# Kernel optimization log

Measured on AMD Instinct MI355X. Metric: run time of the kernel, lower is better.

Reference implementation:

```python
import jax, jax.numpy as jnp
import numpy as np

NUM_BINS = 256


def _per_channel_hist(img):
    # img: [B, C, H, W] with histc range [0, 1].
    B, C, H, W = img.shape
    x = jnp.transpose(img, (1, 0, 2, 3)).reshape(C, -1)  # [C, N]
    # torch.histc: bin = floor(x * bins); value == max goes to last bin;
    # values outside [min, max] are ignored.
    idx = jnp.clip(jnp.floor(x * NUM_BINS).astype(jnp.int32), 0, NUM_BINS - 1)
    valid = ((x >= 0.0) & (x <= 1.0)).astype(img.dtype)  # [C, N]
    offsets = (jnp.arange(C, dtype=jnp.int32) * NUM_BINS)[:, None]
    flat_idx = (idx + offsets).reshape(-1)
    hist = jax.ops.segment_sum(valid.reshape(-1), flat_idx,
                               num_segments=C * NUM_BINS)
    return hist.reshape(C, NUM_BINS)


def setup_inputs() -> dict:
    key = jax.random.key(0)
    k1, k2 = jax.random.split(key)
    img1 = jax.random.uniform(k1, (16, 3, 512, 512), dtype=jnp.float32)
    img2 = jax.random.uniform(k2, (16, 3, 512, 512), dtype=jnp.float32)
    return {"img1": img1, "img2": img2}


def reference(img1, img2):
    h1 = _per_channel_hist(img1)  # [C, bins]
    h2 = _per_channel_hist(img2)
    h1 = h1 / jnp.sum(h1, axis=1, keepdims=True)
    h2 = h2 / jnp.sum(h2, axis=1, keepdims=True)
    cdf1 = jnp.cumsum(h1, axis=1)
    cdf2 = jnp.cumsum(h2, axis=1)
    loss = jnp.sum(jnp.abs(cdf1 - cdf2))  # sum over channels and bins
    return loss / 3.0
```

## Files before the change

kernel.cpp:

```cpp
#include <hip/hip_runtime.h>

#define NUM_BINS 256
#define HW4 65536
#define NGROUPS 6
#define BPG 512
#define GRID (NGROUPS * BPG)
#define THREADS 64
#define F4_PER_BLOCK 2048
#define BATCHES 16
#define ROWS_ALLOC 272

__global__ __launch_bounds__(THREADS) void hist_kernel(
    const float* __restrict__ img1,
    const float* __restrict__ img2,
    unsigned int* __restrict__ ghist ) {

    __shared__ unsigned char h8[ROWS_ALLOC * 64];

    const int lane = threadIdx.x;

    uint4* z = (uint4*)h8;
    #pragma unroll
    for (int i = 0; i < 17; ++i)
        z[i * THREADS + lane] = make_uint4(0u, 0u, 0u, 0u);
    __syncthreads();

    const int gid = blockIdx.x;
    const int group = gid >> 9;
    const int blk = gid & (BPG - 1);
    const int im = (group >= 3) ? 1 : 0;
    const int c = group - im * 3;
    const int b = blk >> 5;
    const int joff = (blk & 31) * F4_PER_BLOCK;
    const float4* __restrict__ src =
        (const float4*)(im ? img2 : img1) + (size_t)(b * 3 + c) * HW4 + joff + lane;

    float4 va = src[0];
    float4 vb = src[THREADS];

    for (int it = 0; it < BATCHES; ++it) {
        float4 na, nb;
        if (it + 1 < BATCHES) {
            na = src[(it + 1) * 2 * THREADS];
            nb = src[(it + 1) * 2 * THREADS + THREADS];
        }

        const float xs[8] = {va.x, va.y, va.z, va.w, vb.x, vb.y, vb.z, vb.w};
        int row[8];
        #pragma unroll
        for (int e = 0; e < 8; ++e) {
            const float x = xs[e];
            int bi = (int)(x * 256.0f);
            bi = bi > (NUM_BINS - 1) ? (NUM_BINS - 1) : bi;
            row[e] = (x >= 0.0f && x <= 1.0f) ? bi : 256;
        }

        unsigned inc[8], dead[8];
        #pragma unroll
        for (int e = 0; e < 8; ++e) { inc[e] = 1u; dead[e] = 0u; }
        #pragma unroll
        for (int i = 0; i < 8; ++i)
            #pragma unroll
            for (int j = i + 1; j < 8; ++j) {
                const unsigned e = (row[i] == row[j]) ? 1u : 0u;
                inc[i] += e;
                dead[j] |= e;
            }

        unsigned v[8];
        #pragma unroll
        for (int e = 0; e < 8; ++e)
            v[e] = h8[(row[e] << 6) | lane];
        #pragma unroll
        for (int e = 0; e < 8; ++e)
            if (!dead[e])
                h8[(row[e] << 6) | lane] = (unsigned char)(v[e] + inc[e]);

        va = na; vb = nb;
    }
    __syncthreads();

    #pragma unroll
    for (int q = 0; q < 4; ++q) {
        const int bin = (q << 6) | lane;
        const unsigned* rowp = (const unsigned*)&h8[bin << 6];
        unsigned s = 0;
        #pragma unroll
        for (int w = 0; w < 16; ++w) {
            const unsigned x = rowp[(w + (lane >> 1)) & 15];
            s += (x & 0xffu) + ((x >> 8) & 0xffu) + ((x >> 16) & 0xffu)
               + (x >> 24);
        }
        if (s) atomicAdd(&ghist[group * NUM_BINS + bin], s);
    }
}

__global__ __launch_bounds__(NUM_BINS) void finalize_kernel(
    const unsigned int* __restrict__ hist, float* __restrict__ out) {

    __shared__ float b1[NUM_BINS];
    __shared__ float b2[NUM_BINS];
    __shared__ float red[NUM_BINS / 64];

    const int t = threadIdx.x;
    float acc = 0.0f;

    for (int c = 0; c < 3; ++c) {
        b1[t] = (float)hist[c * NUM_BINS + t];
        b2[t] = (float)hist[(3 + c) * NUM_BINS + t];
        __syncthreads();
        for (int off = 1; off < NUM_BINS; off <<= 1) {
            float a1 = 0.0f, a2 = 0.0f;
            if (t >= off) { a1 = b1[t - off]; a2 = b2[t - off]; }
            __syncthreads();
            b1[t] += a1;
            b2[t] += a2;
            __syncthreads();
        }
        acc += fabsf(b1[t] / b1[NUM_BINS - 1] - b2[t] / b2[NUM_BINS - 1]);
        __syncthreads();
    }

    #pragma unroll
    for (int off = 32; off > 0; off >>= 1)
        acc += __shfl_down(acc, off, 64);
    if ((t & 63) == 0) red[t >> 6] = acc;
    __syncthreads();
    if (t == 0)
        out[0] = (red[0] + red[1] + red[2] + red[3]) * (1.0f / 3.0f);
}

extern "C" void kernel_launch(void* const* d_in, const int* in_sizes, int n_in,
                              void* d_out, int out_size, void* d_ws,
                              size_t ws_size, hipStream_t stream) {
    const float* img1 = (const float*)d_in[0];
    const float* img2 = (const float*)d_in[1];
    float* out = (float*)d_out;
    unsigned int* hist = (unsigned int*)d_ws;

    hipMemsetAsync(hist, 0, NGROUPS * NUM_BINS * sizeof(unsigned int), stream);

    hist_kernel<<<GRID, THREADS, 0, stream>>>(img1, img2, hist);
    finalize_kernel<<<1, NUM_BINS, 0, stream>>>(hist, out);
}
```

Measured before the change: 140.8 us.

## Use 2D grid with strided chunk distribution, deeper prefetch, and interleaved bin layout

The flat grid of 3072 blocks becomes a 426x6 grid in which each block walks chunks strided by the block count, so each block handles about 20 iterations and fewer blocks are launched. Prefetch depth goes from one to two iterations to hide more load latency. The shared byte histogram pairs adjacent bins per lane so the histogram drops the spill row and fits in 16KB, and out-of-range values now add zero instead of landing in an extra row. The final reduction reads 32 words per stripe and emits two bins each. Uneven per-block work (19 vs 20 iterations) and the extra register pressure are the tradeoffs; 20 increments per lane still fits in an 8-bit counter.

After: 154.7 us. 1.1x slower.

```diff
diff --git a/kernel.cpp b/kernel.cpp
--- a/kernel.cpp
+++ b/kernel.cpp
@@ -3,95 +3,105 @@
 #define NUM_BINS 256
 #define HW4 65536
 #define NGROUPS 6
-#define BPG 512
-#define GRID (NGROUPS * BPG)
+#define BPG 426
+#define CHUNKS 8192
 #define THREADS 64
-#define F4_PER_BLOCK 2048
-#define BATCHES 16
-#define ROWS_ALLOC 272
+#define MAXIT 20
 
 __global__ __launch_bounds__(THREADS) void hist_kernel(
     const float* __restrict__ img1,
     const float* __restrict__ img2,
     unsigned int* __restrict__ ghist ) {
 
-    __shared__ unsigned char h8[ROWS_ALLOC * 64];
+    __shared__ unsigned char h8[16384];
 
     const int lane = threadIdx.x;
+    const int lane2 = lane << 1;
 
     uint4* z = (uint4*)h8;
     #pragma unroll
-    for (int i = 0; i < 17; ++i)
+    for (int i = 0; i < 16; ++i)
         z[i * THREADS + lane] = make_uint4(0u, 0u, 0u, 0u);
     __syncthreads();
 
-    const int gid = blockIdx.x;
-    const int group = gid >> 9;
-    const int blk = gid & (BPG - 1);
+    const int blk = blockIdx.x;
+    const int group = blockIdx.y;
     const int im = (group >= 3) ? 1 : 0;
     const int c = group - im * 3;
-    const int b = blk >> 5;
-    const int joff = (blk & 31) * F4_PER_BLOCK;
-    const float4* __restrict__ src =
-        (const float4*)(im ? img2 : img1) + (size_t)(b * 3 + c) * HW4 + joff + lane;
+    const float4* __restrict__ base = (const float4*)(im ? img2 : img1);
 
-    float4 va = src[0];
-    float4 vb = src[THREADS];
+    const int iters = (blk + (MAXIT - 1) * BPG < CHUNKS) ? MAXIT : (MAXIT - 1);
 
-    for (int it = 0; it < BATCHES; ++it) {
+#define SRC(k) (base + ((size_t)(((k) >> 9) * 3 + c) << 16) + (((k)&511) << 7) + lane)
+
+    float4 va0, vb0, va1, vb1;
+    { const float4* s = SRC(blk); va0 = s[0]; vb0 = s[THREADS]; }
+    if (iters > 1) { const float4* s = SRC(blk + BPG); va1 = s[0]; vb1 = s[THREADS]; }
+
+    for (int it = 0; it < iters; ++it) {
         float4 na, nb;
-        if (it + 1 < BATCHES) {
-            na = src[(it + 1) * 2 * THREADS];
-            nb = src[(it + 1) * 2 * THREADS + THREADS];
+        if (it + 2 < iters) {
+            const float4* s = SRC(blk + (it + 2) * BPG);
+            na = s[0]; nb = s[THREADS];
         }
 
-        const float xs[8] = {va.x, va.y, va.z, va.w, vb.x, vb.y, vb.z, vb.w};
+        const float xs[8] = {va0.x, va0.y, va0.z, va0.w,
+                             vb0.x, vb0.y, vb0.z, vb0.w};
         int row[8];
+        unsigned v0[8];
         #pragma unroll
         for (int e = 0; e < 8; ++e) {
             const float x = xs[e];
             int bi = (int)(x * 256.0f);
-            bi = bi > (NUM_BINS - 1) ? (NUM_BINS - 1) : bi;
-            row[e] = (x >= 0.0f && x <= 1.0f) ? bi : 256;
+            bi = bi < 0 ? 0 : (bi > 255 ? 255 : bi);
+            row[e] = bi;
+            v0[e] = (x >= 0.0f && x <= 1.0f) ? 1u : 0u;
         }
 
         unsigned inc[8], dead[8];
         #pragma unroll
-        for (int e = 0; e < 8; ++e) { inc[e] = 1u; dead[e] = 0u; }
+        for (int e = 0; e < 8; ++e) { inc[e] = v0[e]; dead[e] = 0u; }
         #pragma unroll
         for (int i = 0; i < 8; ++i)
             #pragma unroll
             for (int j = i + 1; j < 8; ++j) {
-                const unsigned e = (row[i] == row[j]) ? 1u : 0u;
-                inc[i] += e;
-                dead[j] |= e;
+                const unsigned m = (row[i] == row[j]) ? 1u : 0u;
+                inc[i] += m & v0[j];
+                dead[j] |= m;
             }
 
+        int a[8];
+        #pragma unroll
+        for (int e = 0; e < 8; ++e)
+            a[e] = (((row[e] >> 1) << 7) | lane2) | (row[e] & 1);
         unsigned v[8];
         #pragma unroll
         for (int e = 0; e < 8; ++e)
-            v[e] = h8[(row[e] << 6) | lane];
+            v[e] = h8[a[e]];
         #pragma unroll
         for (int e = 0; e < 8; ++e)
             if (!dead[e])
-                h8[(row[e] << 6) | lane] = (unsigned char)(v[e] + inc[e]);
+                h8[a[e]] = (unsigned char)(v[e] + inc[e]);
 
-        va = na; vb = nb;
+        va0 = va1; vb0 = vb1; va1 = na; vb1 = nb;
     }
+#undef SRC
     __syncthreads();
 
+    const unsigned* h32 = (const unsigned*)h8;
     #pragma unroll
-    for (int q = 0; q < 4; ++q) {
-        const int bin = (q << 6) | lane;
-        const unsigned* rowp = (const unsigned*)&h8[bin << 6];
-        unsigned s = 0;
+    for (int pass = 0; pass < 2; ++pass) {
+        const int stripe = (pass << 6) | lane;
+        const int wbase = stripe << 5;
+        unsigned s0 = 0, s1 = 0;
         #pragma unroll
-        for (int w = 0; w < 16; ++w) {
-            const unsigned x = rowp[(w + (lane >> 1)) & 15];
-            s += (x & 0xffu) + ((x >> 8) & 0xffu) + ((x >> 16) & 0xffu)
-               + (x >> 24);
+        for (int w = 0; w < 32; ++w) {
+            const unsigned x = h32[wbase + ((w + lane) & 31)];
+            s0 += (x & 0xffu) + ((x >> 16) & 0xffu);
+            s1 += ((x >> 8) & 0xffu) + (x >> 24);
         }
-        if (s) atomicAdd(&ghist[group * NUM_BINS + bin], s);
+        if (s0) atomicAdd(&ghist[group * NUM_BINS + (stripe << 1)], s0);
+        if (s1) atomicAdd(&ghist[group * NUM_BINS + (stripe << 1) + 1], s1);
     }
 }
 
@@ -140,6 +150,7 @@
 
     hipMemsetAsync(hist, 0, NGROUPS * NUM_BINS * sizeof(unsigned int), stream);
 
-    hist_kernel<<<GRID, THREADS, 0, stream>>>(img1, img2, hist);
+    dim3 grid(BPG, NGROUPS);
+    hist_kernel<<<grid, THREADS, 0, stream>>>(img1, img2, hist);
     finalize_kernel<<<1, NUM_BINS, 0, stream>>>(hist, out);
 }
```

## Interleave bin pairs in per-lane byte histogram and simplify conflict handling

Applied to the files above, without the earlier changes.

Changes the per-lane shared-memory byte histogram layout so two adjacent bins share a 2-byte slot per lane, dropping the extra invalid row and shrinking LDS to 16KB. The duplicate-bin handling becomes a prefix count with masked validity, so every element does a store and the dead-flag bookkeeping goes away. The main loop is unrolled by 4, and the final reduction reads 32 words per stripe and emits two bin sums. The goal is fewer LDS bank conflicts and less ALU work, at the cost of redundant stores to the same address within an iteration.

Result: slower. 155.1 us (+10.2%).

```diff
diff --git a/kernel.cpp b/kernel.cpp
--- a/kernel.cpp
+++ b/kernel.cpp
@@ -7,21 +7,21 @@
 #define GRID (NGROUPS * BPG)
 #define THREADS 64
 #define F4_PER_BLOCK 2048
-#define BATCHES 16
-#define ROWS_ALLOC 272
+#define ITERS 16
 
 __global__ __launch_bounds__(THREADS) void hist_kernel(
     const float* __restrict__ img1,
     const float* __restrict__ img2,
     unsigned int* __restrict__ ghist ) {
 
-    __shared__ unsigned char h8[ROWS_ALLOC * 64];
+    __shared__ unsigned char h8[16384];
 
     const int lane = threadIdx.x;
+    const int lane2 = lane << 1;
 
     uint4* z = (uint4*)h8;
     #pragma unroll
-    for (int i = 0; i < 17; ++i)
+    for (int i = 0; i < 16; ++i)
         z[i * THREADS + lane] = make_uint4(0u, 0u, 0u, 0u);
     __syncthreads();
 
@@ -38,60 +38,65 @@
     float4 va = src[0];
     float4 vb = src[THREADS];
 
-    for (int it = 0; it < BATCHES; ++it) {
+    #pragma unroll 4
+    for (int it = 0; it < ITERS; ++it) {
         float4 na, nb;
-        if (it + 1 < BATCHES) {
+        if (it + 1 < ITERS) {
             na = src[(it + 1) * 2 * THREADS];
             nb = src[(it + 1) * 2 * THREADS + THREADS];
         }
 
-        const float xs[8] = {va.x, va.y, va.z, va.w, vb.x, vb.y, vb.z, vb.w};
+        const float xs[8] = {va.x, va.y, va.z, va.w,
+                             vb.x, vb.y, vb.z, vb.w};
         int row[8];
+        unsigned v0[8];
+        int a[8];
         #pragma unroll
         for (int e = 0; e < 8; ++e) {
             const float x = xs[e];
             int bi = (int)(x * 256.0f);
-            bi = bi > (NUM_BINS - 1) ? (NUM_BINS - 1) : bi;
-            row[e] = (x >= 0.0f && x <= 1.0f) ? bi : 256;
+            bi = bi < 0 ? 0 : (bi > 255 ? 255 : bi);
+            row[e] = bi;
+            v0[e] = (x >= 0.0f && x <= 1.0f) ? 1u : 0u;
+            a[e] = ((bi >> 1) << 7) | lane2 | (bi & 1);
         }
-
-        unsigned inc[8], dead[8];
-        #pragma unroll
-        for (int e = 0; e < 8; ++e) { inc[e] = 1u; dead[e] = 0u; }
-        #pragma unroll
-        for (int i = 0; i < 8; ++i)
-            #pragma unroll
-            for (int j = i + 1; j < 8; ++j) {
-                const unsigned e = (row[i] == row[j]) ? 1u : 0u;
-                inc[i] += e;
-                dead[j] |= e;
-            }
 
         unsigned v[8];
         #pragma unroll
         for (int e = 0; e < 8; ++e)
-            v[e] = h8[(row[e] << 6) | lane];
+            v[e] = h8[a[e]];
+
+        unsigned cinc[8];
+        #pragma unroll
+        for (int e = 0; e < 8; ++e) {
+            cinc[e] = v0[e];
+            #pragma unroll
+            for (int j = 0; j < e; ++j)
+                cinc[e] += (row[e] == row[j]) ? v0[j] : 0u;
+        }
+
         #pragma unroll
         for (int e = 0; e < 8; ++e)
-            if (!dead[e])
-                h8[(row[e] << 6) | lane] = (unsigned char)(v[e] + inc[e]);
+            h8[a[e]] = (unsigned char)(v[e] + cinc[e]);
 
         va = na; vb = nb;
     }
     __syncthreads();
 
+    const unsigned* h32 = (const unsigned*)h8;
     #pragma unroll
-    for (int q = 0; q < 4; ++q) {
-        const int bin = (q << 6) | lane;
-        const unsigned* rowp = (const unsigned*)&h8[bin << 6];
-        unsigned s = 0;
+    for (int pass = 0; pass < 2; ++pass) {
+        const int stripe = (pass << 6) | lane;
+        const int wbase = stripe << 5;
+        unsigned s0 = 0, s1 = 0;
         #pragma unroll
-        for (int w = 0; w < 16; ++w) {
-            const unsigned x = rowp[(w + (lane >> 1)) & 15];
-            s += (x & 0xffu) + ((x >> 8) & 0xffu) + ((x >> 16) & 0xffu)
-               + (x >> 24);
+        for (int w = 0; w < 32; ++w) {
+            const unsigned x = h32[wbase + ((w + lane) & 31)];
+            s0 += (x & 0xffu) + ((x >> 16) & 0xffu);
+            s1 += ((x >> 8) & 0xffu) + (x >> 24);
         }
-        if (s) atomicAdd(&ghist[group * NUM_BINS + bin], s);
+        if (s0) atomicAdd(&ghist[group * NUM_BINS + (stripe << 1)], s0);
+        if (s1) atomicAdd(&ghist[group * NUM_BINS + (stripe << 1) + 1], s1);
     }
 }
 
```
